# Performance work log

Measured on AMD Instinct MI355X. Metric: run time of the kernel, lower is better.

Reference implementation:

```python
import jax, jax.numpy as jnp
import numpy as np

T, B, C, H, L = 256, 128, 512, 512, 2
WSCALE = 0.03  # keep gates out of hard saturation


def setup_inputs() -> dict:
    key = jax.random.key(0)
    k1, k2, k3 = jax.random.split(key, 3)
    return {
        "input_tensor": jax.random.normal(k1, (T, B, C), jnp.float32),  # (t, b, c), batch_first=False
        "h0": jnp.zeros((L, 4, B, H), jnp.float32),  # per layer: h, c, h_inner, c_inner
        "Wg": jax.random.normal(k2, (L, 4 * H, C + H), jnp.float32) * WSCALE,  # outer Gates
        "bg": jnp.zeros((L, 4 * H), jnp.float32),
        "Wi": jax.random.normal(k3, (L, 4 * H, 2 * H), jnp.float32) * WSCALE,  # inner LSTMCell Gates
        "bi": jnp.zeros((L, 4 * H), jnp.float32),
    }


def _nested_lstm_layer(x, state, Wg, bg, Wi, bi):
    # x: [T, B, C]; state: (h, c, h_inner, c_inner) each [B, H]
    def step(carry, x_t):
        h, c, hi, ci = carry
        # outer cell gates
        g = jnp.concatenate([x_t, h], axis=1) @ Wg.T + bg  # [B, 4H]
        i, f, o, gc = jnp.split(g, 4, axis=1)
        cell = jax.nn.sigmoid(f) * c + jax.nn.sigmoid(i) * jnp.tanh(gc)
        # inner LSTMCell, input = outer candidate cell
        g2 = jnp.concatenate([cell, hi], axis=1) @ Wi.T + bi  # [B, 4H]
        i2, f2, o2, g2c = jnp.split(g2, 4, axis=1)
        ci_n = jax.nn.sigmoid(f2) * ci + jax.nn.sigmoid(i2) * jnp.tanh(g2c)
        hi_n = jax.nn.sigmoid(o2) * jnp.tanh(ci_n)
        # outer cell state is replaced by inner hidden; outer hidden gated on it
        h_n = jax.nn.sigmoid(o) * jnp.tanh(hi_n)
        return (h_n, hi_n, hi_n, ci_n), h_n

    carry, ys = jax.lax.scan(step, state, x)
    return ys, carry  # ys: [T, B, H]


def reference(input_tensor, h0, Wg, bg, Wi, bi):
    x = input_tensor  # already (t, b, c); scan over leading time axis
    n_layers = Wg.shape[0]
    for l in range(n_layers):
        state = (h0[l, 0], h0[l, 1], h0[l, 2], h0[l, 3])
        x, _ = _nested_lstm_layer(x, state, Wg[l], bg[l], Wi[l], bi[l])
    # return_all_layers=False -> last layer output, shape (t, b, h)
    return x
```

## Files before the change

### kernel.cpp

```cpp
#include <hip/hip_runtime.h>

#define T_DIM 256
#define B_DIM 128
#define C_DIM 512
#define H_DIM 512

typedef _Float16 half8 __attribute__((ext_vector_type(8)));
typedef float f32x4 __attribute__((ext_vector_type(4)));
typedef unsigned u32x4 __attribute__((ext_vector_type(4)));

__device__ __forceinline__ float sigf(float x) { return 1.0f / (1.0f + __expf(-x)); }
__device__ __forceinline__ float tanhf_(float x) {
  float e = __expf(2.0f * x);
  return (e - 1.0f) / (e + 1.0f);
}

__device__ __forceinline__ half8 cvt8(float4 a, float4 b) {
  half8 h;
  h[0] = (_Float16)a.x; h[1] = (_Float16)a.y; h[2] = (_Float16)a.z; h[3] = (_Float16)a.w;
  h[4] = (_Float16)b.x; h[5] = (_Float16)b.y; h[6] = (_Float16)b.z; h[7] = (_Float16)b.w;
  return h;
}

__device__ __forceinline__ void gbar_arrive(unsigned* slots, int bc, unsigned epoch) {
  __syncthreads();
  if (threadIdx.x == 0) *(volatile unsigned*)(slots + bc) = epoch;
}

__device__ __forceinline__ void gbar_wait(const unsigned* slots, unsigned epoch) {
  if (threadIdx.x < 64) {
    const volatile unsigned* myslot =
        (const volatile unsigned*)(slots + (threadIdx.x & 31));
    int guard = 0;
    for (;;) {
      asm volatile("buffer_inv sc0\n\ts_waitcnt vmcnt(0)" ::: "memory");
      unsigned v = *myslot;
      if (__ballot(v >= epoch) == ~0ull) break;
      if (++guard > (1 << 14)) break;
    }
  }
  __syncthreads();
  asm volatile("buffer_inv sc0" ::: "memory");
  asm volatile("s_waitcnt vmcnt(0)" ::: "memory");
}

__device__ __forceinline__ unsigned sysld_u32(const unsigned* p) {
  unsigned v;
  asm volatile("global_load_dword %0, %1, off sc0 sc1\n\ts_waitcnt vmcnt(0)"
               : "=v"(v) : "v"(p) : "memory");
  return v;
}

__device__ __forceinline__ void xpollsys(const unsigned* slots, unsigned epoch) {
  if (threadIdx.x < 64) {
    const unsigned* my = slots + (threadIdx.x & 31);
    int guard = 0;
    for (;;) {
      unsigned v = sysld_u32(my);
      if (__ballot(v >= epoch) == ~0ull) break;
      if (++guard > (1 << 15)) break;
    }
  }
  __syncthreads();
}

__device__ __forceinline__ void xpost(unsigned* flag, unsigned epoch) {
  asm volatile("s_waitcnt vmcnt(0)" ::: "memory");
  asm volatile("global_store_dword %0, %1, off sc0 sc1" ::
                   "v"(flag), "v"(epoch) : "memory");
}

__device__ __forceinline__ void store_llc_h16(_Float16* p, _Float16 v) {
  unsigned u = (unsigned)__builtin_bit_cast(unsigned short, v);
  asm volatile("global_store_short %0, %1, off sc0 sc1" ::
                   "v"(p), "v"(u) : "memory");
}

__global__ __launch_bounds__(256, 1) void nlstm_pipe(
    const float* __restrict__ xin, const float* __restrict__ h0,
    const float* __restrict__ Wg, const float* __restrict__ bgb,
    const float* __restrict__ Wi, const float* __restrict__ bib,
    float* __restrict__ out, unsigned* __restrict__ bar,
    _Float16* __restrict__ y0buf, _Float16* __restrict__ hlcb,
    _Float16* __restrict__ hicb, _Float16* __restrict__ clcb)
{
  __shared__ __align__(16) char smem[65536];
  _Float16* AldsH = (_Float16*)smem;
  float* Pl = (float*)smem;

  const int tid  = threadIdx.x;
  const int xcd  = blockIdx.x & 7;
  const int lyr  = xcd >> 2;
  const int pgrp = xcd & 3;
  const int bc   = blockIdx.x >> 3;
  const int wv   = tid >> 6;
  const int lane = tid & 63;
  const int ln   = lane & 15;
  const int kg   = lane >> 4;
  const int pb   = tid >> 4;
  const int pj   = tid & 15;
  const int jglob = bc * 16 + pj;
  const int ncol  = bc * 16 + ln;
  const int r0    = pgrp * 32;

  const int exo = (jglob >> 5) * 1024 + (((jglob >> 3) & 3) * 16 + pb) * 8 + (jglob & 7);

  unsigned* eslots = bar + xcd * 64;
  unsigned* cslots = eslots + 32;
  unsigned* fwdS = bar + 512 + pgrp * 32;
  unsigned* bakS = bar + 640 + pgrp * 32;

  _Float16* hloc0 = hlcb + ((size_t)xcd * 2 + 0) * 16384;
  _Float16* hloc1 = hlcb + ((size_t)xcd * 2 + 1) * 16384;
  _Float16* hilc0 = hicb + ((size_t)xcd * 2 + 0) * 16384;
  _Float16* hilc1 = hicb + ((size_t)xcd * 2 + 1) * 16384;
  _Float16* cbase = clcb + (size_t)xcd * 16384;
  _Float16* y0s0 = y0buf + ((size_t)pgrp * 2 + 0) * 16384;
  _Float16* y0s1 = y0buf + ((size_t)pgrp * 2 + 1) * 16384;

  half8 wgf[4][8], wif[4][8];
  float bgv[4], biv[4];
#pragma unroll
  for (int g = 0; g < 4; ++g) {
    const float* wgr = Wg + ((size_t)lyr * 2048 + g * 512 + ncol) * 1024 + wv * 256;
    const float* wir = Wi + ((size_t)lyr * 2048 + g * 512 + ncol) * 1024 + wv * 256;
#pragma unroll
    for (int i = 0; i < 8; ++i) {
      const float* p = wgr + i * 32 + kg * 8;
      wgf[g][i] = cvt8(*(const float4*)p, *(const float4*)(p + 4));
      const float* q = wir + i * 32 + kg * 8;
      wif[g][i] = cvt8(*(const float4*)q, *(const float4*)(q + 4));
    }
    bgv[g] = bgb[lyr * 2048 + g * 512 + jglob];
    biv[g] = bib[lyr * 2048 + g * 512 + jglob];
  }

  float st_c[2], st_ci[2], o_pre[2];
  {
    const float* h0l = h0 + (size_t)lyr * 4 * B_DIM * H_DIM + (size_t)(r0 + pb) * H_DIM + jglob;
#pragma unroll
    for (int mt = 0; mt < 2; ++mt) {
      const float* pp = h0l + (size_t)mt * 16 * H_DIM;
      float h_in  = pp[0];
      st_c[mt]    = pp[(size_t)1 * B_DIM * H_DIM];
      float hi_in = pp[(size_t)2 * B_DIM * H_DIM];
      st_ci[mt]   = pp[(size_t)3 * B_DIM * H_DIM];
      hloc0[exo + mt * 512] = (_Float16)h_in;
      hilc0[exo + mt * 512] = (_Float16)hi_in;
      o_pre[mt] = 0.f;
    }
  }

  auto stage_x = [&](int t) {
    const int m = tid & 31;
    const int q = tid >> 5;
    const int mt = m >> 4, mm = m & 15;
    const float* srow = xin + ((size_t)t * B_DIM + r0 + m) * C_DIM;
#pragma unroll
    for (int i = 0; i < 8; ++i) {
      const int chunk = q * 8 + i;
      const int ks = chunk >> 2, kq = chunk & 3;
      const float* p = srow + chunk * 8;
      *(half8*)(AldsH + ks * 1024 + mt * 512 + (kq * 16 + mm) * 8) =
          cvt8(*(const float4*)p, *(const float4*)(p + 4));
    }
  };
  auto copy_slab = [&](int dstHalfBase, const _Float16* src) {
#pragma unroll
    for (int i = 0; i < 8; ++i) {
      const int idx = i * 256 + tid;
      *(u32x4*)(AldsH + dstHalfBase + idx * 8) = *(const u32x4*)(src + idx * 8);
    }
  };
  auto copy_slab_sys = [&](int dstHalfBase, const _Float16* src) {
    u32x4 v[8];
#pragma unroll
    for (int i = 0; i < 8; ++i) {
      const u32x4* p = (const u32x4*)(src + (i * 256 + tid) * 8);
      asm volatile("global_load_dwordx4 %0, %1, off sc0 sc1"
                   : "=v"(v[i]) : "v"(p) : "memory");
    }
    asm volatile("s_waitcnt vmcnt(0)" ::: "memory");
    __builtin_amdgcn_sched_barrier(0);
#pragma unroll
    for (int i = 0; i < 8; ++i)
      *(u32x4*)(AldsH + dstHalfBase + (i * 256 + tid) * 8) = v[i];
  };
  auto gemm = [&](half8 (&wf)[4][8]) {
    f32x4 acc[2][4];
#pragma unroll
    for (int mt = 0; mt < 2; ++mt)
#pragma unroll
      for (int g = 0; g < 4; ++g) acc[mt][g] = (f32x4){0.f, 0.f, 0.f, 0.f};
#pragma unroll
    for (int i = 0; i < 8; ++i) {
      const _Float16* ab = AldsH + (wv * 8 + i) * 1024 + lane * 8;
      half8 a0 = *(const half8*)(ab);
      half8 a1 = *(const half8*)(ab + 512);
#pragma unroll
      for (int g = 0; g < 4; ++g) {
        acc[0][g] = __builtin_amdgcn_mfma_f32_16x16x32_f16(a0, wf[g][i], acc[0][g], 0, 0, 0);
        acc[1][g] = __builtin_amdgcn_mfma_f32_16x16x32_f16(a1, wf[g][i], acc[1][g], 0, 0, 0);
      }
    }
    __syncthreads();
#pragma unroll
    for (int mt = 0; mt < 2; ++mt)
#pragma unroll
      for (int g = 0; g < 4; ++g)
#pragma unroll
        for (int rr = 0; rr < 4; ++rr)
          Pl[(((g * 2 + mt) * 16 + kg * 4 + rr) * 16 + ln) * 4 + (wv ^ kg)] = acc[mt][g][rr];
    __syncthreads();
  };
  auto plsum = [&](int g, int mt) -> float {
    f32x4 v = *(const f32x4*)(Pl + (((g * 2 + mt) * 16 + pb) * 16 + pj) * 4);
    return v[0] + v[1] + v[2] + v[3];
  };

  unsigned eseq = 0, cseq = 0;

  gbar_arrive(eslots, bc, ++eseq);
  if (lyr == 0) stage_x(0);
  gbar_wait(eslots, eseq);
  if (lyr == 1) {
    xpollsys(fwdS, 1u);
    copy_slab_sys(0, y0s1);
    __syncthreads();
    if (tid == 0) xpost(bakS + bc, 1u);
  }

  for (int t = 0; t < T_DIM; ++t) {
    const int pr = t & 1;
    _Float16* hrd  = pr ? hloc1 : hloc0;
    _Float16* hwr  = pr ? hloc0 : hloc1;
    _Float16* hird = pr ? hilc1 : hilc0;
    _Float16* hiwr = pr ? hilc0 : hilc1;
    _Float16* y0wr = pr ? y0s0 : y0s1;
    _Float16* y0rd = pr ? y0s1 : y0s0;

    copy_slab(16384, hrd);
    __syncthreads();

    gemm(wgf);

#pragma unroll
    for (int mt = 0; mt < 2; ++mt) {
      float gi = plsum(0, mt) + bgv[0];
      float gf = plsum(1, mt) + bgv[1];
      float go = plsum(2, mt) + bgv[2];
      float gc = plsum(3, mt) + bgv[3];
      float cell = sigf(gf) * st_c[mt] + sigf(gi) * tanhf_(gc);
      o_pre[mt] = go;
      cbase[exo + mt * 512] = (_Float16)cell;
    }
    gbar_arrive(cslots, bc, ++cseq);
    copy_slab(16384, hird);
    gbar_wait(cslots, cseq);

    copy_slab(0, cbase);
    __syncthreads();

    gemm(wif);

#pragma unroll
    for (int mt = 0; mt < 2; ++mt) {
      float i2 = plsum(0, mt) + biv[0];
      float f2 = plsum(1, mt) + biv[1];
      float o2 = plsum(2, mt) + biv[2];
      float c2 = plsum(3, mt) + biv[3];
      float ci_n = sigf(f2) * st_ci[mt] + sigf(i2) * tanhf_(c2);
      float hi_n = sigf(o2) * tanhf_(ci_n);
      float h_n  = sigf(o_pre[mt]) * tanhf_(hi_n);
      st_ci[mt] = ci_n;
      st_c[mt]  = hi_n;
      hiwr[exo + mt * 512] = (_Float16)hi_n;
      hwr[exo + mt * 512]  = (_Float16)h_n;
      if (lyr == 0) {
        store_llc_h16(y0wr + exo + mt * 512, (_Float16)h_n);
      } else {
        out[((size_t)t * B_DIM + (r0 + pb + mt * 16)) * H_DIM + jglob] = h_n;
      }
    }

    gbar_arrive(eslots, bc, ++eseq);
    if (lyr == 0) {
      if (tid == 0) xpost(fwdS + bc, (unsigned)(t + 1));
      if (t + 1 < T_DIM) stage_x(t + 1);
      if (t >= 1 && t + 1 < T_DIM) xpollsys(bakS, (unsigned)t);
    } else if (t + 1 < T_DIM) {
      xpollsys(fwdS, (unsigned)(t + 2));
      copy_slab_sys(0, y0rd);
      __syncthreads();
      if (tid == 0) xpost(bakS + bc, (unsigned)(t + 2));
    }
    gbar_wait(eslots, eseq);
  }
}

extern "C" void kernel_launch(void* const* d_in, const int* in_sizes, int n_in,
                              void* d_out, int out_size, void* d_ws, size_t ws_size,
                              hipStream_t stream) {
  const float* xin = (const float*)d_in[0];
  const float* h0  = (const float*)d_in[1];
  const float* Wg  = (const float*)d_in[2];
  const float* bg  = (const float*)d_in[3];
  const float* Wi  = (const float*)d_in[4];
  const float* bi  = (const float*)d_in[5];
  float* out = (float*)d_out;

  unsigned* bar  = (unsigned*)d_ws;
  _Float16* y0b  = (_Float16*)((char*)d_ws + 4096);
  _Float16* hlcb = y0b + (size_t)4 * 2 * 16384;
  _Float16* hicb = hlcb + (size_t)8 * 2 * 16384;
  _Float16* clcb = hicb + (size_t)8 * 2 * 16384;

  hipMemsetAsync(d_ws, 0, 4096, stream);

  nlstm_pipe<<<dim3(256), dim3(256), 0, stream>>>(
      xin, h0, Wg, bg, Wi, bi, out, bar, y0b, hlcb, hicb, clcb);
}
```

Baseline: 2.695 ms.

## Split gate GEMMs by K-half across waves to overlap with barrier waits

Splits each step's gate GEMMs along K. Waves 0-1 handle the input half (x or the outer cell) and waves 2-3 handle the recurrent half (h or h_inner), with partial sums written to a dedicated LDS region. The input-half GEMM for the next step now runs right after x/y0 staging, before the grid barrier wait. The h_inner GEMM runs between the cell-barrier arrive and wait, so MFMA work overlaps the cross-block synchronisation. It also enlarges the layer-0 to layer-1 y0 ring from 2 to 4 slots, which loosens the back-pressure polling, and assigns polling to specific waves. The costs are a doubled LDS footprint, extra __syncthreads, and more intricate ordering that could hide races.

```diff
diff --git a/kernel.cpp b/kernel.cpp
--- a/kernel.cpp
+++ b/kernel.cpp
@@ -4,6 +4,11 @@
 #define B_DIM 128
 #define C_DIM 512
 #define H_DIM 512
+
+#define R0H 0
+#define R1H 16384
+#define R2H 32768
+#define PLB 98304
 
 typedef _Float16 half8 __attribute__((ext_vector_type(8)));
 typedef float f32x4 __attribute__((ext_vector_type(4)));
@@ -27,8 +32,9 @@
   if (threadIdx.x == 0) *(volatile unsigned*)(slots + bc) = epoch;
 }
 
-__device__ __forceinline__ void gbar_wait(const unsigned* slots, unsigned epoch) {
-  if (threadIdx.x < 64) {
+__device__ __forceinline__ void gbar_wait_pw(const unsigned* slots, unsigned epoch,
+                                             int pollwave) {
+  if ((int)(threadIdx.x >> 6) == pollwave) {
     const volatile unsigned* myslot =
         (const volatile unsigned*)(slots + (threadIdx.x & 31));
     int guard = 0;
@@ -51,17 +57,14 @@
   return v;
 }
 
-__device__ __forceinline__ void xpollsys(const unsigned* slots, unsigned epoch) {
-  if (threadIdx.x < 64) {
-    const unsigned* my = slots + (threadIdx.x & 31);
-    int guard = 0;
-    for (;;) {
-      unsigned v = sysld_u32(my);
-      if (__ballot(v >= epoch) == ~0ull) break;
-      if (++guard > (1 << 15)) break;
-    }
-  }
-  __syncthreads();
+__device__ __forceinline__ void xpoll_raw(const unsigned* slots, unsigned epoch) {
+  const unsigned* my = slots + (threadIdx.x & 31);
+  int guard = 0;
+  for (;;) {
+    unsigned v = sysld_u32(my);
+    if (__ballot(v >= epoch) == ~0ull) break;
+    if (++guard > (1 << 15)) break;
+  }
 }
 
 __device__ __forceinline__ void xpost(unsigned* flag, unsigned epoch) {
@@ -84,9 +87,9 @@
     _Float16* __restrict__ y0buf, _Float16* __restrict__ hlcb,
     _Float16* __restrict__ hicb, _Float16* __restrict__ clcb)
 {
-  __shared__ __align__(16) char smem[65536];
+  __shared__ __align__(16) char smem[131072];
   _Float16* AldsH = (_Float16*)smem;
-  float* Pl = (float*)smem;
+  float* Pl = (float*)(smem + PLB);
 
   const int tid  = threadIdx.x;
   const int xcd  = blockIdx.x & 7;
@@ -115,8 +118,7 @@
   _Float16* hilc0 = hicb + ((size_t)xcd * 2 + 0) * 16384;
   _Float16* hilc1 = hicb + ((size_t)xcd * 2 + 1) * 16384;
   _Float16* cbase = clcb + (size_t)xcd * 16384;
-  _Float16* y0s0 = y0buf + ((size_t)pgrp * 2 + 0) * 16384;
-  _Float16* y0s1 = y0buf + ((size_t)pgrp * 2 + 1) * 16384;
+  _Float16* y0base = y0buf + (size_t)pgrp * 4 * 16384;
 
   half8 wgf[4][8], wif[4][8];
   float bgv[4], biv[4];
@@ -161,18 +163,29 @@
       const int chunk = q * 8 + i;
       const int ks = chunk >> 2, kq = chunk & 3;
       const float* p = srow + chunk * 8;
-      *(half8*)(AldsH + ks * 1024 + mt * 512 + (kq * 16 + mm) * 8) =
+      *(half8*)(AldsH + R0H + ks * 1024 + mt * 512 + (kq * 16 + mm) * 8) =
           cvt8(*(const float4*)p, *(const float4*)(p + 4));
     }
   };
-  auto copy_slab = [&](int dstHalfBase, const _Float16* src) {
-#pragma unroll
-    for (int i = 0; i < 8; ++i) {
-      const int idx = i * 256 + tid;
-      *(u32x4*)(AldsH + dstHalfBase + idx * 8) = *(const u32x4*)(src + idx * 8);
-    }
-  };
-  auto copy_slab_sys = [&](int dstHalfBase, const _Float16* src) {
+  auto copy_hhi = [&](const _Float16* hrd, const _Float16* hird) {
+    u32x4 vh[8], vy[8];
+#pragma unroll
+    for (int i = 0; i < 8; ++i) vh[i] = *(const u32x4*)(hrd + (i * 256 + tid) * 8);
+#pragma unroll
+    for (int i = 0; i < 8; ++i) vy[i] = *(const u32x4*)(hird + (i * 256 + tid) * 8);
+#pragma unroll
+    for (int i = 0; i < 8; ++i) *(u32x4*)(AldsH + R1H + (i * 256 + tid) * 8) = vh[i];
+#pragma unroll
+    for (int i = 0; i < 8; ++i) *(u32x4*)(AldsH + R2H + (i * 256 + tid) * 8) = vy[i];
+  };
+  auto copy_r0 = [&](const _Float16* src) {
+    u32x4 v[8];
+#pragma unroll
+    for (int i = 0; i < 8; ++i) v[i] = *(const u32x4*)(src + (i * 256 + tid) * 8);
+#pragma unroll
+    for (int i = 0; i < 8; ++i) *(u32x4*)(AldsH + R0H + (i * 256 + tid) * 8) = v[i];
+  };
+  auto copy_r0_sys = [&](const _Float16* src) {
     u32x4 v[8];
 #pragma unroll
     for (int i = 0; i < 8; ++i) {
@@ -184,17 +197,12 @@
     __builtin_amdgcn_sched_barrier(0);
 #pragma unroll
     for (int i = 0; i < 8; ++i)
-      *(u32x4*)(AldsH + dstHalfBase + (i * 256 + tid) * 8) = v[i];
-  };
-  auto gemm = [&](half8 (&wf)[4][8]) {
-    f32x4 acc[2][4];
-#pragma unroll
-    for (int mt = 0; mt < 2; ++mt)
-#pragma unroll
-      for (int g = 0; g < 4; ++g) acc[mt][g] = (f32x4){0.f, 0.f, 0.f, 0.f};
+      *(u32x4*)(AldsH + R0H + (i * 256 + tid) * 8) = v[i];
+  };
+  auto mfma8 = [&](const _Float16* rb, int ksb, half8 (&wf)[4][8], f32x4 (&acc)[2][4]) {
 #pragma unroll
     for (int i = 0; i < 8; ++i) {
-      const _Float16* ab = AldsH + (wv * 8 + i) * 1024 + lane * 8;
+      const _Float16* ab = rb + (ksb + i) * 1024 + lane * 8;
       half8 a0 = *(const half8*)(ab);
       half8 a1 = *(const half8*)(ab + 512);
 #pragma unroll
@@ -203,7 +211,8 @@
         acc[1][g] = __builtin_amdgcn_mfma_f32_16x16x32_f16(a1, wf[g][i], acc[1][g], 0, 0, 0);
       }
     }
-    __syncthreads();
+  };
+  auto plw = [&](f32x4 (&acc)[2][4]) {
 #pragma unroll
     for (int mt = 0; mt < 2; ++mt)
 #pragma unroll
@@ -211,7 +220,6 @@
 #pragma unroll
         for (int rr = 0; rr < 4; ++rr)
           Pl[(((g * 2 + mt) * 16 + kg * 4 + rr) * 16 + ln) * 4 + (wv ^ kg)] = acc[mt][g][rr];
-    __syncthreads();
   };
   auto plsum = [&](int g, int mt) -> float {
     f32x4 v = *(const f32x4*)(Pl + (((g * 2 + mt) * 16 + pb) * 16 + pj) * 4);
@@ -222,12 +230,22 @@
 
   gbar_arrive(eslots, bc, ++eseq);
   if (lyr == 0) stage_x(0);
-  gbar_wait(eslots, eseq);
+  gbar_wait_pw(eslots, eseq, 3);
   if (lyr == 1) {
-    xpollsys(fwdS, 1u);
-    copy_slab_sys(0, y0s1);
+    if (wv == 0) xpoll_raw(fwdS, 1u);
+    __syncthreads();
+    copy_r0_sys(y0base + 0);
     __syncthreads();
     if (tid == 0) xpost(bakS + bc, 1u);
+  }
+  if (wv < 2) {
+    f32x4 acc[2][4];
+#pragma unroll
+    for (int mt = 0; mt < 2; ++mt)
+#pragma unroll
+      for (int g = 0; g < 4; ++g) acc[mt][g] = (f32x4){0.f, 0.f, 0.f, 0.f};
+    mfma8(AldsH + R0H, 8 * wv, wgf, acc);
+    plw(acc);
   }
 
   for (int t = 0; t < T_DIM; ++t) {
@@ -236,13 +254,22 @@
     _Float16* hwr  = pr ? hloc0 : hloc1;
     _Float16* hird = pr ? hilc1 : hilc0;
     _Float16* hiwr = pr ? hilc0 : hilc1;
-    _Float16* y0wr = pr ? y0s0 : y0s1;
-    _Float16* y0rd = pr ? y0s1 : y0s0;
-
-    copy_slab(16384, hrd);
-    __syncthreads();
-
-    gemm(wgf);
+    _Float16* y0wr = y0base + (size_t)(t & 3) * 16384;
+    _Float16* y0rd = y0base + (size_t)((t + 1) & 3) * 16384;
+
+    copy_hhi(hrd, hird);
+    __syncthreads();
+
+    if (wv >= 2) {
+      f32x4 acc[2][4];
+#pragma unroll
+      for (int mt = 0; mt < 2; ++mt)
+#pragma unroll
+        for (int g = 0; g < 4; ++g) acc[mt][g] = (f32x4){0.f, 0.f, 0.f, 0.f};
+      mfma8(AldsH + R1H, 8 * wv - 16, wgf, acc);
+      plw(acc);
+    }
+    __syncthreads();
 
 #pragma unroll
     for (int mt = 0; mt < 2; ++mt) {
@@ -255,13 +282,30 @@
       cbase[exo + mt * 512] = (_Float16)cell;
     }
     gbar_arrive(cslots, bc, ++cseq);
-    copy_slab(16384, hird);
-    gbar_wait(cslots, cseq);
-
-    copy_slab(0, cbase);
-    __syncthreads();
-
-    gemm(wif);
+    if (wv >= 2) {
+      f32x4 acc[2][4];
+#pragma unroll
+      for (int mt = 0; mt < 2; ++mt)
+#pragma unroll
+        for (int g = 0; g < 4; ++g) acc[mt][g] = (f32x4){0.f, 0.f, 0.f, 0.f};
+      mfma8(AldsH + R2H, 8 * wv - 16, wif, acc);
+      plw(acc);
+    }
+    gbar_wait_pw(cslots, cseq, 0);
+
+    copy_r0(cbase);
+    __syncthreads();
+
+    if (wv < 2) {
+      f32x4 acc[2][4];
+#pragma unroll
+      for (int mt = 0; mt < 2; ++mt)
+#pragma unroll
+        for (int g = 0; g < 4; ++g) acc[mt][g] = (f32x4){0.f, 0.f, 0.f, 0.f};
+      mfma8(AldsH + R0H, 8 * wv, wif, acc);
+      plw(acc);
+    }
+    __syncthreads();
 
 #pragma unroll
     for (int mt = 0; mt < 2; ++mt) {
@@ -286,15 +330,38 @@
     gbar_arrive(eslots, bc, ++eseq);
     if (lyr == 0) {
       if (tid == 0) xpost(fwdS + bc, (unsigned)(t + 1));
-      if (t + 1 < T_DIM) stage_x(t + 1);
-      if (t >= 1 && t + 1 < T_DIM) xpollsys(bakS, (unsigned)t);
+      if (t + 1 < T_DIM) {
+        stage_x(t + 1);
+        __syncthreads();
+        if (wv < 2) {
+          f32x4 acc[2][4];
+#pragma unroll
+          for (int mt = 0; mt < 2; ++mt)
+#pragma unroll
+            for (int g = 0; g < 4; ++g) acc[mt][g] = (f32x4){0.f, 0.f, 0.f, 0.f};
+          mfma8(AldsH + R0H, 8 * wv, wgf, acc);
+          plw(acc);
+        } else if (wv == 3 && t >= 2) {
+          xpoll_raw(bakS, (unsigned)(t - 2));
+        }
+      }
     } else if (t + 1 < T_DIM) {
-      xpollsys(fwdS, (unsigned)(t + 2));
-      copy_slab_sys(0, y0rd);
+      if (wv == 0) xpoll_raw(fwdS, (unsigned)(t + 2));
+      __syncthreads();
+      copy_r0_sys(y0rd);
       __syncthreads();
       if (tid == 0) xpost(bakS + bc, (unsigned)(t + 2));
-    }
-    gbar_wait(eslots, eseq);
+      if (wv < 2) {
+        f32x4 acc[2][4];
+#pragma unroll
+        for (int mt = 0; mt < 2; ++mt)
+#pragma unroll
+          for (int g = 0; g < 4; ++g) acc[mt][g] = (f32x4){0.f, 0.f, 0.f, 0.f};
+        mfma8(AldsH + R0H, 8 * wv, wgf, acc);
+        plw(acc);
+      }
+    }
+    gbar_wait_pw(eslots, eseq, 3);
   }
 }
 
@@ -311,7 +378,7 @@
 
   unsigned* bar  = (unsigned*)d_ws;
   _Float16* y0b  = (_Float16*)((char*)d_ws + 4096);
-  _Float16* hlcb = y0b + (size_t)4 * 2 * 16384;
+  _Float16* hlcb = y0b + (size_t)4 * 4 * 16384;
   _Float16* hicb = hlcb + (size_t)8 * 2 * 16384;
   _Float16* clcb = hicb + (size_t)8 * 2 * 16384;
 
```

Measured after the change: 2.412 ms. 10.5% less time.
